# Performance work log

Measured on AMD Instinct MI355X. Metric: run time of the kernel, lower is better.

The kernel has to match this reference:

```python
import jax, jax.numpy as jnp
import numpy as np
import math

N_HEADS = 8
EMB = 128
KEY_DIM = EMB // N_HEADS  # 16
B, NQ, T = 32, 1024, 1024


def _uniform(key, shape, stdv):
    return jax.random.uniform(key, shape, jnp.float32, -stdv, stdv)


def setup_inputs() -> dict:
    key = jax.random.key(0)
    ks = jax.random.split(key, 7)
    stdv = 1.0 / math.sqrt(KEY_DIM)      # last dim of w_query/w_key/w_value
    stdv_o = 1.0 / math.sqrt(EMB)        # last dim of w_out
    q = jax.random.normal(ks[0], (B, NQ, EMB), jnp.float32)
    h = jax.random.normal(ks[1], (B, T, EMB), jnp.float32)
    mask = jax.random.randint(ks[2], (B, NQ, T), 0, 2).astype(bool)
    return {
        "q": q,
        "h": h,
        "mask": mask,
        "w_query": _uniform(ks[3], (N_HEADS, EMB, KEY_DIM), stdv),
        "w_key": _uniform(ks[4], (N_HEADS, EMB, KEY_DIM), stdv),
        "w_value": _uniform(ks[5], (N_HEADS, EMB, KEY_DIM), stdv),
        "w_out": _uniform(ks[6], (N_HEADS, KEY_DIM, EMB), stdv_o),
    }


def reference(q, h, mask, w_query, w_key, w_value, w_out):
    # q: [B, NQ, E], h: [B, T, E], mask: [B, NQ, T] (True = blocked)
    scale = 1.0 / math.sqrt(KEY_DIM)
    Q = jnp.einsum('bqi,hik->hbqk', q, w_query)   # [H,B,NQ,dk]
    K = jnp.einsum('bti,hik->hbtk', h, w_key)     # [H,B,T,dk]
    V = jnp.einsum('bti,hiv->hbtv', h, w_value)   # [H,B,T,dv]
    U = scale * jnp.einsum('hbqk,hbtk->hbqt', Q, K)  # [H,B,NQ,T]
    m = mask[None]                                   # broadcast over heads
    U = jnp.where(m, -jnp.inf, U)
    attn = jax.nn.softmax(U, axis=-1)
    attn = jnp.where(m, 0.0, attn)                   # explicit zeroing as in original
    heads = jnp.einsum('hbqt,hbtv->hbqv', attn, V)   # [H,B,NQ,dv]
    out = jnp.einsum('hbqv,hve->bqe', heads, w_out)  # [B,NQ,E]
    return out
```

## Files before the change

### kernel.cpp

```cpp
#include <hip/hip_runtime.h>
#include <hip/hip_bf16.h>
#include <stdint.h>


typedef __attribute__((ext_vector_type(8))) short bf16x8;
typedef __attribute__((ext_vector_type(4))) float f32x4;
typedef __attribute__((ext_vector_type(16))) float f32x16;

#define NEGBIG (-1e30f)
#define QSCALE 0.36067376022224085f
#define EXP2(x) __builtin_amdgcn_exp2f(x)
#define PSTRIDE 68

__device__ __forceinline__ unsigned short f2bf(float x) {
  union { __hip_bfloat16 h; unsigned short u; } cv;
  cv.h = __float2bfloat16(x);
  return cv.u;
}
__device__ __forceinline__ unsigned int pk2bf(float a, float b) {
  unsigned int ua = __float_as_uint(a) + 0x8000u;
  unsigned int ub = __float_as_uint(b) + 0x8000u;
  return __builtin_amdgcn_perm(ub, ua, 0x07060302u);
}

__global__ __launch_bounds__(256) void maskpack_k(const void* __restrict__ mask,
                                                  unsigned long long* __restrict__ mp64) {
  __shared__ unsigned short mlds[256];
  const int tid = threadIdx.x;
  const unsigned int* mi = (const unsigned int*)mask;
  unsigned int acc = 0;
  #pragma unroll
  for (int k = 0; k < 16; ++k) acc |= mi[k * 251];
  const bool bytemode = acc > 1u;

  const long long i0 = ((long long)blockIdx.x * 256 + tid) * 16;
  unsigned int v = 0;
  if (bytemode) {
    int4 w = *(const int4*)((const unsigned char*)mask + i0);
    unsigned int ws[4] = {(unsigned)w.x, (unsigned)w.y, (unsigned)w.z, (unsigned)w.w};
    #pragma unroll
    for (int d = 0; d < 4; ++d)
      #pragma unroll
      for (int j = 0; j < 4; ++j)
        v |= (((ws[d] >> (8*j)) & 0xFFu) ? 1u : 0u) << (d*4 + j);
  } else {
    const int4* mp = (const int4*)((const int*)mask + i0);
    #pragma unroll
    for (int d = 0; d < 4; ++d) {
      int4 w = mp[d];
      v |= (w.x ? 1u : 0u) << (d*4 + 0);
      v |= (w.y ? 1u : 0u) << (d*4 + 1);
      v |= (w.z ? 1u : 0u) << (d*4 + 2);
      v |= (w.w ? 1u : 0u) << (d*4 + 3);
    }
  }
  mlds[tid] = (unsigned short)v;
  __syncthreads();
  if (tid < 64)
    mp64[(long long)blockIdx.x * 64 + tid] = ((const unsigned long long*)mlds)[tid];
}

__global__ __launch_bounds__(256) void projqkv_k(const float* __restrict__ qp,
                                                 const float* __restrict__ hp,
                                                 const float* __restrict__ wqp,
                                                 const float* __restrict__ wkp,
                                                 const float* __restrict__ wvp,
                                                 unsigned short* __restrict__ Qb,
                                                 unsigned short* __restrict__ Kb,
                                                 unsigned short* __restrict__ Vt) {
  __shared__ unsigned short WtLds[128 * 136];
  __shared__ __align__(16) unsigned short Cxf[9216];
  const int tid = threadIdx.x;
  const int wave = tid >> 6, lane = tid & 63;
  const int llo4 = lane & 15, lhi4 = lane >> 4;
  const int m0 = blockIdx.x * 64;
  const int b = m0 >> 10, row0 = m0 & 1023;
  const int sel = blockIdx.y;
  const float* A = (sel == 0) ? qp : hp;
  const float* W = (sel == 0) ? wqp : (sel == 1) ? wkp : wvp;
  const float wscale = (sel == 0) ? QSCALE : 1.0f;

  #pragma unroll
  for (int i = 0; i < 8; ++i) {
    int base = (tid + i * 256) * 8;
    float4 w0 = *(const float4*)&W[base];
    float4 w1 = *(const float4*)&W[base + 4];
    float wv8[8] = {w0.x, w0.y, w0.z, w0.w, w1.x, w1.y, w1.z, w1.w};
    #pragma unroll
    for (int j = 0; j < 8; ++j) {
      int idx = base + j;
      int h = idx >> 11, e = (idx >> 4) & 127, kk = idx & 15;
      WtLds[(h*16 + kk) * 136 + e] = f2bf(wv8[j] * wscale);
    }
  }
  #pragma unroll
  for (int i = 0; i < 4; ++i) {
    int r = (tid >> 4) + i * 16;
    int c = (tid & 15) * 8;
    float4 a0 = *(const float4*)&A[(m0 + r) * 128 + c];
    float4 a1 = *(const float4*)&A[(m0 + r) * 128 + c + 4];
    bf16x8 a8;
    a8[0] = (short)f2bf(a0.x); a8[1] = (short)f2bf(a0.y);
    a8[2] = (short)f2bf(a0.z); a8[3] = (short)f2bf(a0.w);
    a8[4] = (short)f2bf(a1.x); a8[5] = (short)f2bf(a1.y);
    a8[6] = (short)f2bf(a1.z); a8[7] = (short)f2bf(a1.w);
    *(bf16x8*)&Cxf[r * 136 + c] = a8;
  }
  __syncthreads();

  const int n0 = wave * 32;
  f32x4 acc[4][2] = {};
  #pragma unroll
  for (int kk = 0; kk < 128; kk += 32) {
    bf16x8 af[4], bfr[2];
    #pragma unroll
    for (int mi2 = 0; mi2 < 4; ++mi2)
      af[mi2] = *(const bf16x8*)&Cxf[(mi2*16 + llo4)*136 + kk + lhi4*8];
    #pragma unroll
    for (int ni = 0; ni < 2; ++ni)
      bfr[ni] = *(const bf16x8*)&WtLds[(n0 + ni*16 + llo4)*136 + kk + lhi4*8];
    #pragma unroll
    for (int mi2 = 0; mi2 < 4; ++mi2)
      #pragma unroll
      for (int ni = 0; ni < 2; ++ni)
        acc[mi2][ni] = __builtin_amdgcn_mfma_f32_16x16x32_bf16(af[mi2], bfr[ni], acc[mi2][ni], 0, 0, 0);
  }

  __syncthreads();
  if (sel < 2) {
    unsigned short* Cb = sel ? Kb : Qb;
    #pragma unroll
    for (int mi2 = 0; mi2 < 4; ++mi2)
      #pragma unroll
      for (int ni = 0; ni < 2; ++ni) {
        int n = n0 + ni*16 + llo4;
        #pragma unroll
        for (int r = 0; r < 4; ++r)
          Cxf[(mi2*16 + lhi4*4 + r)*136 + n] = f2bf(acc[mi2][ni][r]);
      }
    __syncthreads();
    #pragma unroll
    for (int it = 0; it < 4; ++it) {
      int u = tid + it*256;
      int h = u >> 7, rk = u & 127, row = rk >> 1, kh = rk & 1;
      bf16x8 vv = *(const bf16x8*)&Cxf[row*136 + h*16 + kh*8];
      *(bf16x8*)&Cb[((b*8 + h)*1024 + row0 + row)*16 + kh*8] = vv;
    }
  } else {
    #pragma unroll
    for (int mi2 = 0; mi2 < 4; ++mi2)
      #pragma unroll
      for (int ni = 0; ni < 2; ++ni) {
        int n = n0 + ni*16 + llo4;
        ushort4 pk;
        pk.x = f2bf(acc[mi2][ni][0]); pk.y = f2bf(acc[mi2][ni][1]);
        pk.z = f2bf(acc[mi2][ni][2]); pk.w = f2bf(acc[mi2][ni][3]);
        *(ushort4*)&Cxf[n*72 + mi2*16 + lhi4*4] = pk;
      }
    __syncthreads();
    #pragma unroll
    for (int it = 0; it < 4; ++it) {
      int u = tid + it*256;
      int n = u >> 3, tc = u & 7;
      int h = n >> 4, k = n & 15;
      bf16x8 vv = *(const bf16x8*)&Cxf[n*72 + tc*8];
      *(bf16x8*)&Vt[((b*8 + h)*16 + k)*1024 + row0 + tc*8] = vv;
    }
  }
}

__global__ __launch_bounds__(256) void attn_k(const unsigned short* __restrict__ Qb,
                                              const unsigned short* __restrict__ Kb,
                                              const unsigned short* __restrict__ Vtb,
                                              const unsigned long long* __restrict__ mp64,
                                              unsigned short* __restrict__ heads) {
  __shared__ __align__(16) unsigned short Plds[4][32 * PSTRIDE];
  __shared__ __align__(8) uint2 mlut[16];
  const int tid = threadIdx.x;
  const int wave = tid >> 6, lane = tid & 63;
  const int llo4 = lane & 15, lhi4 = lane >> 4;
  const int llo5 = lane & 31, lhi5 = lane >> 5;
  const int q0 = blockIdx.x * 128 + wave * 32;
  const int b  = blockIdx.y;
  const int h  = blockIdx.z;
  const int bh = b * 8 + h;
  unsigned short* Pw = &Plds[wave][0];
  const unsigned long long* mp_base = &mp64[((b << 10) + q0 + llo5) * 16];
  const unsigned short* Kbase = &Kb[(bh * 1024 + llo5) * 16 + lhi5 * 8];
  const unsigned short* Vbase = &Vtb[(bh * 16 + llo4) * 1024 + lhi4 * 8];

  if (tid < 16) {
    unsigned int n = tid;
    unsigned int h0 = (n & 1u) ? 0u : 0xFFFFu;
    unsigned int h1 = (n & 2u) ? 0u : 0xFFFFu;
    unsigned int h2 = (n & 4u) ? 0u : 0xFFFFu;
    unsigned int h3 = (n & 8u) ? 0u : 0xFFFFu;
    mlut[tid] = make_uint2(h0 | (h1 << 16), h2 | (h3 << 16));
  }
  __syncthreads();

  bf16x8 qf = *(const bf16x8*)&Qb[(bh * 1024 + q0 + llo5) * 16 + lhi5 * 8];

  bf16x8 ones;
  #pragma unroll
  for (int j = 0; j < 8; ++j) ones[j] = (short)0x3F80;
  f32x16 cb16;
  #pragma unroll
  for (int j = 0; j < 16; ++j) cb16[j] = -18.f;

  f32x4 ot[2] = {};
  f32x4 lacc[2] = {};

  bf16x8 kfb[2][2], vfb[2][2];
  unsigned long long mwb[2];

  #pragma unroll
  for (int tt = 0; tt < 2; ++tt)
    kfb[0][tt] = *(const bf16x8*)&Kbase[(tt*32) * 16];
  #pragma unroll
  for (int kt = 0; kt < 2; ++kt)
    vfb[0][kt] = *(const bf16x8*)&Vbase[kt*32];
  mwb[0] = mp_base[0];

  #pragma unroll 2
  for (int tw = 0; tw < 16; ++tw) {
    const int cur = tw & 1, nxt = cur ^ 1;
    const int twn = (tw < 15) ? tw + 1 : 15;
    const int t0n = twn * 64;
    #pragma unroll
    for (int tt = 0; tt < 2; ++tt)
      kfb[nxt][tt] = *(const bf16x8*)&Kbase[(t0n + tt*32) * 16];
    #pragma unroll
    for (int kt = 0; kt < 2; ++kt)
      vfb[nxt][kt] = *(const bf16x8*)&Vbase[t0n + kt*32];
    mwb[nxt] = mp_base[twn];

    f32x16 st[2];
    #pragma unroll
    for (int tt = 0; tt < 2; ++tt)
      st[tt] = __builtin_amdgcn_mfma_f32_32x32x16_bf16(kfb[cur][tt], qf, cb16, 0, 0, 0);

    const unsigned int mwlo = (unsigned int)mwb[cur];
    const unsigned int mwhi = (unsigned int)(mwb[cur] >> 32);
    #pragma unroll
    for (int tt = 0; tt < 2; ++tt) {
      const unsigned int m32 = (tt ? mwhi : mwlo) >> (lhi5 * 4);
      #pragma unroll
      for (int g = 0; g < 4; ++g) {
        unsigned int nib = (m32 >> (g*8)) & 0xFu;
        uint2 am = mlut[nib];
        uint2 d;
        d.x = pk2bf(EXP2(st[tt][g*4 + 0]), EXP2(st[tt][g*4 + 1])) & am.x;
        d.y = pk2bf(EXP2(st[tt][g*4 + 2]), EXP2(st[tt][g*4 + 3])) & am.y;
        *(uint2*)&Pw[llo5 * PSTRIDE + tt*32 + lhi5*4 + g*8] = d;
      }
    }

    #pragma unroll
    for (int kt = 0; kt < 2; ++kt) {
      #pragma unroll
      for (int qn = 0; qn < 2; ++qn) {
        const unsigned short* pp = &Pw[(qn*16 + llo4) * PSTRIDE + kt*32 + lhi4*8];
        uint2 p0 = *(const uint2*)pp;
        uint2 p1 = *(const uint2*)(pp + 4);
        union { uint2 u[2]; bf16x8 v; } pf;
        pf.u[0] = p0; pf.u[1] = p1;
        ot[qn]   = __builtin_amdgcn_mfma_f32_16x16x32_bf16(vfb[cur][kt], pf.v, ot[qn], 0, 0, 0);
        lacc[qn] = __builtin_amdgcn_mfma_f32_16x16x32_bf16(ones,        pf.v, lacc[qn], 0, 0, 0);
      }
    }
  }

  #pragma unroll
  for (int qn = 0; qn < 2; ++qn) {
    float l = lacc[qn][0];
    float inv = l > 0.f ? 1.f / l : 0.f;
    f32x4 o = ot[qn] * inv;
    uint2 d;
    d.x = pk2bf(o[0], o[1]);
    d.y = pk2bf(o[2], o[3]);
    *(uint2*)&heads[((b << 10) + q0 + qn*16 + llo4) * 128 + h*16 + lhi4*4] = d;
  }
}

__global__ __launch_bounds__(256) void outproj_k(const unsigned short* __restrict__ Av,
                                                 const float* __restrict__ W,
                                                 float* __restrict__ Co) {
  __shared__ unsigned short WtLds[128 * 136];
  __shared__ __align__(16) unsigned short Cxf[9216];
  const int tid = threadIdx.x;
  const int wave = tid >> 6, lane = tid & 63;
  const int llo4 = lane & 15, lhi4 = lane >> 4;
  const int m0 = blockIdx.x * 64;

  #pragma unroll
  for (int i = 0; i < 8; ++i) {
    int base = (tid + i * 256) * 8;
    float4 w0 = *(const float4*)&W[base];
    float4 w1 = *(const float4*)&W[base + 4];
    float wv8[8] = {w0.x, w0.y, w0.z, w0.w, w1.x, w1.y, w1.z, w1.w};
    #pragma unroll
    for (int j = 0; j < 8; ++j) {
      int idx = base + j;
      WtLds[(idx & 127) * 136 + (idx >> 7)] = f2bf(wv8[j]);
    }
  }
  #pragma unroll
  for (int i = 0; i < 4; ++i) {
    int r = (tid >> 4) + i * 16;
    int c = (tid & 15) * 8;
    *(bf16x8*)&Cxf[r * 136 + c] = *(const bf16x8*)&Av[(m0 + r) * 128 + c];
  }
  __syncthreads();

  const int n0 = wave * 32;
  f32x4 acc[4][2] = {};
  #pragma unroll
  for (int kk = 0; kk < 128; kk += 32) {
    bf16x8 af[4], bfr[2];
    #pragma unroll
    for (int mi2 = 0; mi2 < 4; ++mi2)
      af[mi2] = *(const bf16x8*)&Cxf[(mi2*16 + llo4)*136 + kk + lhi4*8];
    #pragma unroll
    for (int ni = 0; ni < 2; ++ni)
      bfr[ni] = *(const bf16x8*)&WtLds[(n0 + ni*16 + llo4)*136 + kk + lhi4*8];
    #pragma unroll
    for (int mi2 = 0; mi2 < 4; ++mi2)
      #pragma unroll
      for (int ni = 0; ni < 2; ++ni)
        acc[mi2][ni] = __builtin_amdgcn_mfma_f32_16x16x32_bf16(af[mi2], bfr[ni], acc[mi2][ni], 0, 0, 0);
  }
  #pragma unroll
  for (int mi2 = 0; mi2 < 4; ++mi2)
    #pragma unroll
    for (int ni = 0; ni < 2; ++ni) {
      int n = n0 + ni*16 + llo4;
      int mbase = m0 + mi2*16 + lhi4*4;
      #pragma unroll
      for (int r = 0; r < 4; ++r)
        Co[(mbase + r) * 128 + n] = acc[mi2][ni][r];
    }
}

extern "C" void kernel_launch(void* const* d_in, const int* in_sizes, int n_in,
                              void* d_out, int out_size, void* d_ws, size_t ws_size,
                              hipStream_t stream) {
  const float* q  = (const float*)d_in[0];
  const float* hh = (const float*)d_in[1];
  const void*  mk = d_in[2];
  const float* wq = (const float*)d_in[3];
  const float* wk = (const float*)d_in[4];
  const float* wv = (const float*)d_in[5];
  const float* wo = (const float*)d_in[6];
  float* out = (float*)d_out;

  unsigned short* Qb = (unsigned short*)d_ws;
  unsigned short* Kb = Qb + 32*8*1024*16;
  unsigned short* Vt = Kb + 32*8*1024*16;
  unsigned short* hd = Vt + 32*8*1024*16;
  unsigned long long* mp64 = (unsigned long long*)(hd + 32768*128);

  maskpack_k<<<8192, 256, 0, stream>>>(mk, mp64);
  projqkv_k<<<dim3(512, 3), 256, 0, stream>>>(q, hh, wq, wk, wv, Qb, Kb, Vt);
  attn_k<<<dim3(8, 32, 8), 256, 0, stream>>>(Qb, Kb, Vt, mp64, hd);
  outproj_k<<<512, 256, 0, stream>>>(hd, wo, out);
}
```

Measured before the change: 306.9 us.

## Fuse mask packing into attention kernel and share mask tile across heads

Removes the separate mask-packing kernel and its workspace round trip. The attention kernel now packs the 32-row mask tile straight from global memory into LDS. The grid is regrouped so each block covers 32 queries across all 8 heads, with each wave doing 2 heads in sequence, so the mask is read once per block and reused across heads. This cuts a kernel launch and the bitmask write/read. In exchange, per-wave parallelism drops to 32 query rows with a serial head loop, and each block has a mask-load prologue before compute starts.

New measurement: 304.9 us. About the same (-0.6%).

```diff
diff --git a/kernel.cpp b/kernel.cpp
--- a/kernel.cpp
+++ b/kernel.cpp
@@ -21,43 +21,6 @@
   unsigned int ua = __float_as_uint(a) + 0x8000u;
   unsigned int ub = __float_as_uint(b) + 0x8000u;
   return __builtin_amdgcn_perm(ub, ua, 0x07060302u);
-}
-
-__global__ __launch_bounds__(256) void maskpack_k(const void* __restrict__ mask,
-                                                  unsigned long long* __restrict__ mp64) {
-  __shared__ unsigned short mlds[256];
-  const int tid = threadIdx.x;
-  const unsigned int* mi = (const unsigned int*)mask;
-  unsigned int acc = 0;
-  #pragma unroll
-  for (int k = 0; k < 16; ++k) acc |= mi[k * 251];
-  const bool bytemode = acc > 1u;
-
-  const long long i0 = ((long long)blockIdx.x * 256 + tid) * 16;
-  unsigned int v = 0;
-  if (bytemode) {
-    int4 w = *(const int4*)((const unsigned char*)mask + i0);
-    unsigned int ws[4] = {(unsigned)w.x, (unsigned)w.y, (unsigned)w.z, (unsigned)w.w};
-    #pragma unroll
-    for (int d = 0; d < 4; ++d)
-      #pragma unroll
-      for (int j = 0; j < 4; ++j)
-        v |= (((ws[d] >> (8*j)) & 0xFFu) ? 1u : 0u) << (d*4 + j);
-  } else {
-    const int4* mp = (const int4*)((const int*)mask + i0);
-    #pragma unroll
-    for (int d = 0; d < 4; ++d) {
-      int4 w = mp[d];
-      v |= (w.x ? 1u : 0u) << (d*4 + 0);
-      v |= (w.y ? 1u : 0u) << (d*4 + 1);
-      v |= (w.z ? 1u : 0u) << (d*4 + 2);
-      v |= (w.w ? 1u : 0u) << (d*4 + 3);
-    }
-  }
-  mlds[tid] = (unsigned short)v;
-  __syncthreads();
-  if (tid < 64)
-    mp64[(long long)blockIdx.x * 64 + tid] = ((const unsigned long long*)mlds)[tid];
 }
 
 __global__ __launch_bounds__(256) void projqkv_k(const float* __restrict__ qp,
@@ -172,22 +135,18 @@
 __global__ __launch_bounds__(256) void attn_k(const unsigned short* __restrict__ Qb,
                                               const unsigned short* __restrict__ Kb,
                                               const unsigned short* __restrict__ Vtb,
-                                              const unsigned long long* __restrict__ mp64,
+                                              const void* __restrict__ mask,
                                               unsigned short* __restrict__ heads) {
   __shared__ __align__(16) unsigned short Plds[4][32 * PSTRIDE];
+  __shared__ __align__(8) unsigned short Mlds[32 * PSTRIDE];
   __shared__ __align__(8) uint2 mlut[16];
   const int tid = threadIdx.x;
   const int wave = tid >> 6, lane = tid & 63;
   const int llo4 = lane & 15, lhi4 = lane >> 4;
   const int llo5 = lane & 31, lhi5 = lane >> 5;
-  const int q0 = blockIdx.x * 128 + wave * 32;
+  const int q0 = blockIdx.x * 32;
   const int b  = blockIdx.y;
-  const int h  = blockIdx.z;
-  const int bh = b * 8 + h;
   unsigned short* Pw = &Plds[wave][0];
-  const unsigned long long* mp_base = &mp64[((b << 10) + q0 + llo5) * 16];
-  const unsigned short* Kbase = &Kb[(bh * 1024 + llo5) * 16 + lhi5 * 8];
-  const unsigned short* Vbase = &Vtb[(bh * 16 + llo4) * 1024 + lhi4 * 8];
 
   if (tid < 16) {
     unsigned int n = tid;
@@ -197,9 +156,44 @@
     unsigned int h3 = (n & 8u) ? 0u : 0xFFFFu;
     mlut[tid] = make_uint2(h0 | (h1 << 16), h2 | (h3 << 16));
   }
+
+  {
+    const unsigned int* mi32 = (const unsigned int*)mask;
+    unsigned int accv = 0;
+    #pragma unroll
+    for (int k = 0; k < 16; ++k) accv |= mi32[k * 251];
+    const bool bytemode = accv > 1u;
+
+    const int crow = tid >> 6;
+    const int cchk = tid & 63;
+    #pragma unroll
+    for (int i = 0; i < 8; ++i) {
+      const int qrow = crow + i * 4;
+      const long long base = ((long long)((b << 10) + q0 + qrow) << 10) + cchk * 16;
+      unsigned int v = 0;
+      if (bytemode) {
+        int4 w = *(const int4*)((const unsigned char*)mask + base);
+        unsigned int ws[4] = {(unsigned)w.x, (unsigned)w.y, (unsigned)w.z, (unsigned)w.w};
+        #pragma unroll
+        for (int d = 0; d < 4; ++d)
+          #pragma unroll
+          for (int j = 0; j < 4; ++j)
+            v |= (((ws[d] >> (8*j)) & 0xFFu) ? 1u : 0u) << (d*4 + j);
+      } else {
+        const int4* mp4 = (const int4*)((const int*)mask + base);
+        #pragma unroll
+        for (int d = 0; d < 4; ++d) {
+          int4 w = mp4[d];
+          v |= (w.x ? 1u : 0u) << (d*4 + 0);
+          v |= (w.y ? 1u : 0u) << (d*4 + 1);
+          v |= (w.z ? 1u : 0u) << (d*4 + 2);
+          v |= (w.w ? 1u : 0u) << (d*4 + 3);
+        }
+      }
+      Mlds[qrow * PSTRIDE + cchk] = (unsigned short)v;
+    }
+  }
   __syncthreads();
-
-  bf16x8 qf = *(const bf16x8*)&Qb[(bh * 1024 + q0 + llo5) * 16 + lhi5 * 8];
 
   bf16x8 ones;
   #pragma unroll
@@ -208,78 +202,87 @@
   #pragma unroll
   for (int j = 0; j < 16; ++j) cb16[j] = -18.f;
 
-  f32x4 ot[2] = {};
-  f32x4 lacc[2] = {};
-
-  bf16x8 kfb[2][2], vfb[2][2];
-  unsigned long long mwb[2];
-
-  #pragma unroll
-  for (int tt = 0; tt < 2; ++tt)
-    kfb[0][tt] = *(const bf16x8*)&Kbase[(tt*32) * 16];
-  #pragma unroll
-  for (int kt = 0; kt < 2; ++kt)
-    vfb[0][kt] = *(const bf16x8*)&Vbase[kt*32];
-  mwb[0] = mp_base[0];
-
-  #pragma unroll 2
-  for (int tw = 0; tw < 16; ++tw) {
-    const int cur = tw & 1, nxt = cur ^ 1;
-    const int twn = (tw < 15) ? tw + 1 : 15;
-    const int t0n = twn * 64;
+  for (int hh = 0; hh < 2; ++hh) {
+    const int h  = wave * 2 + hh;
+    const int bh = b * 8 + h;
+    const unsigned short* Kbase = &Kb[(bh * 1024 + llo5) * 16 + lhi5 * 8];
+    const unsigned short* Vbase = &Vtb[(bh * 16 + llo4) * 1024 + lhi4 * 8];
+
+    bf16x8 qf = *(const bf16x8*)&Qb[(bh * 1024 + q0 + llo5) * 16 + lhi5 * 8];
+
+    f32x4 ot[2] = {};
+    f32x4 lacc[2] = {};
+
+    bf16x8 kfb[2][2], vfb[2][2];
+    unsigned long long mwb[2];
+
     #pragma unroll
     for (int tt = 0; tt < 2; ++tt)
-      kfb[nxt][tt] = *(const bf16x8*)&Kbase[(t0n + tt*32) * 16];
+      kfb[0][tt] = *(const bf16x8*)&Kbase[(tt*32) * 16];
     #pragma unroll
     for (int kt = 0; kt < 2; ++kt)
-      vfb[nxt][kt] = *(const bf16x8*)&Vbase[t0n + kt*32];
-    mwb[nxt] = mp_base[twn];
-
-    f32x16 st[2];
-    #pragma unroll
-    for (int tt = 0; tt < 2; ++tt)
-      st[tt] = __builtin_amdgcn_mfma_f32_32x32x16_bf16(kfb[cur][tt], qf, cb16, 0, 0, 0);
-
-    const unsigned int mwlo = (unsigned int)mwb[cur];
-    const unsigned int mwhi = (unsigned int)(mwb[cur] >> 32);
-    #pragma unroll
-    for (int tt = 0; tt < 2; ++tt) {
-      const unsigned int m32 = (tt ? mwhi : mwlo) >> (lhi5 * 4);
-      #pragma unroll
-      for (int g = 0; g < 4; ++g) {
-        unsigned int nib = (m32 >> (g*8)) & 0xFu;
-        uint2 am = mlut[nib];
-        uint2 d;
-        d.x = pk2bf(EXP2(st[tt][g*4 + 0]), EXP2(st[tt][g*4 + 1])) & am.x;
-        d.y = pk2bf(EXP2(st[tt][g*4 + 2]), EXP2(st[tt][g*4 + 3])) & am.y;
-        *(uint2*)&Pw[llo5 * PSTRIDE + tt*32 + lhi5*4 + g*8] = d;
-      }
-    }
-
-    #pragma unroll
-    for (int kt = 0; kt < 2; ++kt) {
-      #pragma unroll
-      for (int qn = 0; qn < 2; ++qn) {
-        const unsigned short* pp = &Pw[(qn*16 + llo4) * PSTRIDE + kt*32 + lhi4*8];
-        uint2 p0 = *(const uint2*)pp;
-        uint2 p1 = *(const uint2*)(pp + 4);
-        union { uint2 u[2]; bf16x8 v; } pf;
-        pf.u[0] = p0; pf.u[1] = p1;
-        ot[qn]   = __builtin_amdgcn_mfma_f32_16x16x32_bf16(vfb[cur][kt], pf.v, ot[qn], 0, 0, 0);
-        lacc[qn] = __builtin_amdgcn_mfma_f32_16x16x32_bf16(ones,        pf.v, lacc[qn], 0, 0, 0);
-      }
-    }
-  }
-
-  #pragma unroll
-  for (int qn = 0; qn < 2; ++qn) {
-    float l = lacc[qn][0];
-    float inv = l > 0.f ? 1.f / l : 0.f;
-    f32x4 o = ot[qn] * inv;
-    uint2 d;
-    d.x = pk2bf(o[0], o[1]);
-    d.y = pk2bf(o[2], o[3]);
-    *(uint2*)&heads[((b << 10) + q0 + qn*16 + llo4) * 128 + h*16 + lhi4*4] = d;
+      vfb[0][kt] = *(const bf16x8*)&Vbase[kt*32];
+    mwb[0] = *(const unsigned long long*)&Mlds[llo5 * PSTRIDE];
+
+    #pragma unroll 2
+    for (int tw = 0; tw < 16; ++tw) {
+      const int cur = tw & 1, nxt = cur ^ 1;
+      const int twn = (tw < 15) ? tw + 1 : 15;
+      const int t0n = twn * 64;
+      #pragma unroll
+      for (int tt = 0; tt < 2; ++tt)
+        kfb[nxt][tt] = *(const bf16x8*)&Kbase[(t0n + tt*32) * 16];
+      #pragma unroll
+      for (int kt = 0; kt < 2; ++kt)
+        vfb[nxt][kt] = *(const bf16x8*)&Vbase[t0n + kt*32];
+      mwb[nxt] = *(const unsigned long long*)&Mlds[llo5 * PSTRIDE + twn * 4];
+
+      f32x16 st[2];
+      #pragma unroll
+      for (int tt = 0; tt < 2; ++tt)
+        st[tt] = __builtin_amdgcn_mfma_f32_32x32x16_bf16(kfb[cur][tt], qf, cb16, 0, 0, 0);
+
+      const unsigned int mwlo = (unsigned int)mwb[cur];
+      const unsigned int mwhi = (unsigned int)(mwb[cur] >> 32);
+      #pragma unroll
+      for (int tt = 0; tt < 2; ++tt) {
+        const unsigned int m32 = (tt ? mwhi : mwlo) >> (lhi5 * 4);
+        #pragma unroll
+        for (int g = 0; g < 4; ++g) {
+          unsigned int nib = (m32 >> (g*8)) & 0xFu;
+          uint2 am = mlut[nib];
+          uint2 d;
+          d.x = pk2bf(EXP2(st[tt][g*4 + 0]), EXP2(st[tt][g*4 + 1])) & am.x;
+          d.y = pk2bf(EXP2(st[tt][g*4 + 2]), EXP2(st[tt][g*4 + 3])) & am.y;
+          *(uint2*)&Pw[llo5 * PSTRIDE + tt*32 + lhi5*4 + g*8] = d;
+        }
+      }
+
+      #pragma unroll
+      for (int kt = 0; kt < 2; ++kt) {
+        #pragma unroll
+        for (int qn = 0; qn < 2; ++qn) {
+          const unsigned short* pp = &Pw[(qn*16 + llo4) * PSTRIDE + kt*32 + lhi4*8];
+          uint2 p0 = *(const uint2*)pp;
+          uint2 p1 = *(const uint2*)(pp + 4);
+          union { uint2 u[2]; bf16x8 v; } pf;
+          pf.u[0] = p0; pf.u[1] = p1;
+          ot[qn]   = __builtin_amdgcn_mfma_f32_16x16x32_bf16(vfb[cur][kt], pf.v, ot[qn], 0, 0, 0);
+          lacc[qn] = __builtin_amdgcn_mfma_f32_16x16x32_bf16(ones,        pf.v, lacc[qn], 0, 0, 0);
+        }
+      }
+    }
+
+    #pragma unroll
+    for (int qn = 0; qn < 2; ++qn) {
+      float l = lacc[qn][0];
+      float inv = l > 0.f ? 1.f / l : 0.f;
+      f32x4 o = ot[qn] * inv;
+      uint2 d;
+      d.x = pk2bf(o[0], o[1]);
+      d.y = pk2bf(o[2], o[3]);
+      *(uint2*)&heads[((b << 10) + q0 + qn*16 + llo4) * 128 + h*16 + lhi4*4] = d;
+    }
   }
 }
 
@@ -358,10 +361,8 @@
   unsigned short* Kb = Qb + 32*8*1024*16;
   unsigned short* Vt = Kb + 32*8*1024*16;
   unsigned short* hd = Vt + 32*8*1024*16;
-  unsigned long long* mp64 = (unsigned long long*)(hd + 32768*128);
-
-  maskpack_k<<<8192, 256, 0, stream>>>(mk, mp64);
+
   projqkv_k<<<dim3(512, 3), 256, 0, stream>>>(q, hh, wq, wk, wv, Qb, Kb, Vt);
-  attn_k<<<dim3(8, 32, 8), 256, 0, stream>>>(Qb, Kb, Vt, mp64, hd);
+  attn_k<<<dim3(32, 32), 256, 0, stream>>>(Qb, Kb, Vt, mk, hd);
   outproj_k<<<512, 256, 0, stream>>>(hd, wo, out);
 }
```
